# Optimization experiments

Measured on AMD Instinct MI355X. Metric: run time of the kernel, lower is better.

The kernel has to match this reference:

```python
import jax, jax.numpy as jnp
import numpy as np
import math

HIDDEN = 1024
HEADS = 16
HEAD_DIM = HIDDEN // HEADS


def setup_inputs() -> dict:
    key = jax.random.key(0)
    ks = jax.random.split(key, 9)
    s = 1.0 / math.sqrt(HIDDEN)
    x = jax.random.normal(ks[0], (4, 2048, HIDDEN), dtype=jnp.float32)
    Wq = jax.random.uniform(ks[1], (HIDDEN, HIDDEN), jnp.float32, -s, s)
    bq = jax.random.uniform(ks[2], (HIDDEN,), jnp.float32, -s, s)
    Wk = jax.random.uniform(ks[3], (HIDDEN, HIDDEN), jnp.float32, -s, s)
    bk = jax.random.uniform(ks[4], (HIDDEN,), jnp.float32, -s, s)
    Wv = jax.random.uniform(ks[5], (HIDDEN, HIDDEN), jnp.float32, -s, s)
    bv = jax.random.uniform(ks[6], (HIDDEN,), jnp.float32, -s, s)
    Wo = jax.random.uniform(ks[7], (HIDDEN, HIDDEN), jnp.float32, -s, s)
    bo = jax.random.uniform(ks[8], (HIDDEN,), jnp.float32, -s, s)
    return {"x": x, "Wq": Wq, "bq": bq, "Wk": Wk, "bk": bk,
            "Wv": Wv, "bv": bv, "Wo": Wo, "bo": bo}


def reference(x, Wq, bq, Wk, bk, Wv, bv, Wo, bo):
    B, T, D = x.shape
    H, Hd = HEADS, HEAD_DIM
    scale = 1.0 / math.sqrt(Hd)
    # projections (torch Linear: y = x @ W.T + b)
    q = (x @ Wq.T + bq).reshape(B, T, H, Hd).transpose(0, 2, 1, 3)  # [B,H,T,Hd]
    k = (x @ Wk.T + bk).reshape(B, T, H, Hd).transpose(0, 2, 1, 3)
    v = (x @ Wv.T + bv).reshape(B, T, H, Hd).transpose(0, 2, 1, 3)
    scores = jnp.einsum("bhqd,bhkd->bhqk", q, k) * scale  # [B,H,T,T]
    attn = jax.nn.softmax(scores, axis=-1)
    out = jnp.einsum("bhqk,bhkd->bhqd", attn, v)  # [B,H,T,Hd]
    out = out.transpose(0, 2, 1, 3).reshape(B, T, D)
    out = out @ Wo.T + bo
    return out.mean(axis=1)  # [B, D]
```

## Files before the change

kernel.cpp:

```cpp
#include <hip/hip_runtime.h>
#include <stdint.h>

#define HIDDEN 1024
#define HEADS 16
#define HEAD_DIM 64
#define BATCH 4
#define SEQ 2048
#define NTOK (BATCH * SEQ)

typedef __attribute__((ext_vector_type(8))) short bf16x8;
typedef __attribute__((ext_vector_type(4))) float floatx4;
typedef __attribute__((ext_vector_type(16))) float floatx16;

#define SCALE_Q 0.18033688011112042f

__device__ __forceinline__ unsigned short f2bf(float f) {
    union { float f; unsigned u; } x; x.f = f;
    unsigned r = x.u + 0x7fffu + ((x.u >> 16) & 1u);
    return (unsigned short)(r >> 16);
}

__device__ __forceinline__ float fast_exp2(float x) {
#if __has_builtin(__builtin_amdgcn_exp2f)
    return __builtin_amdgcn_exp2f(x);
#else
    return exp2f(x);
#endif
}

typedef __attribute__((address_space(3))) unsigned int lds_u32;
typedef const __attribute__((address_space(1))) unsigned int gl_u32;

__device__ __forceinline__ void async_cp16(const void* g, void* l) {
#if __has_builtin(__builtin_amdgcn_global_load_lds)
    __builtin_amdgcn_global_load_lds((gl_u32*)g, (lds_u32*)l, 16, 0, 0);
#else
    *(uint4*)((char*)l + (threadIdx.x & 63) * 16) = *(const uint4*)g;
#endif
}

__global__ __launch_bounds__(256) void conv_all(
    const float* __restrict__ x, const float* __restrict__ Wq,
    const float* __restrict__ Wk, const float* __restrict__ Wv,
    unsigned short* __restrict__ x_bf, unsigned short* __restrict__ wq_bf,
    unsigned short* __restrict__ wk_bf, unsigned short* __restrict__ wv_bf,
    float* __restrict__ accp) {
    const int blk = blockIdx.x, tid = threadIdx.x;
    const float* src;
    unsigned short* dst;
    size_t i;
    if (blk < 8192) {
        src = x; dst = x_bf; i = (size_t)blk * 256 + tid;
        if (blk < 16) accp[blk * 256 + tid] = 0.0f;
    } else {
        int r = blk - 8192;
        int s = r >> 10;
        src = (s == 0) ? Wq : (s == 1) ? Wk : Wv;
        dst = (s == 0) ? wq_bf : (s == 1) ? wk_bf : wv_bf;
        i = (size_t)(r & 1023) * 256 + tid;
    }
    float4 v = *(const float4*)(src + 4 * i);
    unsigned short o[4];
    o[0] = f2bf(v.x); o[1] = f2bf(v.y); o[2] = f2bf(v.z); o[3] = f2bf(v.w);
    *(ushort4*)(dst + 4 * i) = *(ushort4*)o;
}

__global__ __launch_bounds__(256, 3) void qkv_gemm(
    const unsigned short* __restrict__ X,
    const unsigned short* __restrict__ W0, const unsigned short* __restrict__ W1,
    const unsigned short* __restrict__ W2,
    const float* __restrict__ b0, const float* __restrict__ b1,
    const float* __restrict__ b2,
    unsigned short* __restrict__ O0, unsigned short* __restrict__ O1,
    unsigned short* __restrict__ O2) {
    __shared__ __align__(16) char smem[34816];
    unsigned short* tbuf = (unsigned short*)smem;

    const int id = blockIdx.x;
    const int mb = id & 63, nzb = id >> 6;
    const int z = nzb >> 3, nz = nzb & 7;
    const int m0 = mb * 128;
    const unsigned short* W = (z == 0) ? W0 : (z == 1) ? W1 : W2;
    const float* bias       = (z == 0) ? b0 : (z == 1) ? b1 : b2;

    const int tid = threadIdx.x, lane = tid & 63, wave = tid >> 6;
    const int wm = (wave & 1) * 64, wn = (wave >> 1) * 64;

    const int srow = lane >> 2;
    const int sxc = ((lane & 3) ^ (srow & 3)) * 8;
    const unsigned short* ga[2];
    const unsigned short* gb[2];
#pragma unroll
    for (int j = 0; j < 2; ++j) {
        ga[j] = X + (size_t)(m0 + wave * 32 + j * 16 + srow) * HIDDEN + sxc;
        gb[j] = W + (size_t)(nz * 128 + wave * 32 + j * 16 + srow) * HIDDEN + sxc;
    }

    floatx4 acc[4][4];
#pragma unroll
    for (int tm = 0; tm < 4; ++tm)
#pragma unroll
        for (int tn = 0; tn < 4; ++tn)
#pragma unroll
            for (int r = 0; r < 4; ++r) acc[tm][tn][r] = 0.f;

#pragma unroll
    for (int j = 0; j < 2; ++j) {
        async_cp16(ga[j], smem + wave * 2048 + j * 1024);
        async_cp16(gb[j], smem + 16384 + wave * 2048 + j * 1024);
        ga[j] += 32; gb[j] += 32;
    }
    __syncthreads();

    const int fr = (lane & 15) * 64 + (((lane >> 4) ^ (lane & 3)) * 16);
    for (int kt = 0; kt < 32; ++kt) {
        const int cur = kt & 1;
        if (kt < 31) {
#pragma unroll
            for (int j = 0; j < 2; ++j) {
                async_cp16(ga[j], smem + (cur ^ 1) * 8192 + wave * 2048 + j * 1024);
                async_cp16(gb[j], smem + 16384 + (cur ^ 1) * 8192 + wave * 2048 + j * 1024);
                ga[j] += 32; gb[j] += 32;
            }
        }
        const char* Ab = smem + cur * 8192;
        const char* Bb = smem + 16384 + cur * 8192;
        bf16x8 af[4], bfr[4];
#pragma unroll
        for (int t = 0; t < 4; ++t) {
            af[t]  = *(bf16x8*)(Ab + (wm + t * 16) * 64 + fr);
            bfr[t] = *(bf16x8*)(Bb + (wn + t * 16) * 64 + fr);
        }
#pragma unroll
        for (int tm = 0; tm < 4; ++tm)
#pragma unroll
            for (int tn = 0; tn < 4; ++tn)
                acc[tm][tn] = __builtin_amdgcn_mfma_f32_16x16x32_bf16(af[tm], bfr[tn], acc[tm][tn], 0, 0, 0);
        if (kt < 31) __syncthreads();
    }

    const int col = lane & 15, rbase = (lane >> 4) * 4;
    __syncthreads();
    if (z == 2) {
#pragma unroll
        for (int tm = 0; tm < 4; ++tm)
#pragma unroll
            for (int tn = 0; tn < 4; ++tn) {
                const int dr = wn + tn * 16 + col;
                const float bs = bias[nz * 128 + dr];
                const int mi0 = wm + tm * 16 + rbase;
                const int mip = (mi0 & ~12) | ((mi0 & 4) << 1) | ((mi0 & 8) >> 1);
                unsigned short vals[4];
#pragma unroll
                for (int r = 0; r < 4; ++r) vals[r] = f2bf(acc[tm][tn][r] + bs);
                *(ushort4*)&tbuf[dr * 136 + mip] = *(ushort4*)vals;
            }
        __syncthreads();
        const int dr = tid >> 1, seg = tid & 1;
        const int hh = nz * 2 + (dr >> 6), dd = dr & 63;
        const int bb = m0 >> 11, tb = (m0 & (SEQ - 1)) >> 7;
        unsigned short* dst = O2 + (((size_t)bb * HEADS + hh) * HEAD_DIM + dd) * SEQ
                                 + tb * 128 + seg * 64;
        const unsigned short* srcl = &tbuf[dr * 136 + seg * 64];
#pragma unroll
        for (int i = 0; i < 8; ++i)
            *(uint4*)(dst + i * 8) = *(const uint4*)(srcl + i * 8);
    } else {
        unsigned short* O = (z == 0) ? O0 : O1;
        const float sc = (z == 0) ? SCALE_Q : 1.0f;
#pragma unroll
        for (int tm = 0; tm < 4; ++tm)
#pragma unroll
            for (int tn = 0; tn < 4; ++tn) {
                const int nn = wn + tn * 16 + col;
                const float bs = bias[nz * 128 + nn];
                const int mi0 = wm + tm * 16 + rbase;
#pragma unroll
                for (int r = 0; r < 4; ++r)
                    tbuf[(mi0 + r) * 136 + nn] = f2bf((acc[tm][tn][r] + bs) * sc);
            }
        __syncthreads();
        const int r = tid >> 1, seg = tid & 1;
        unsigned short* dst = O + (size_t)(m0 + r) * HIDDEN + nz * 128 + seg * 64;
        const unsigned short* srcl = &tbuf[r * 136 + seg * 64];
#pragma unroll
        for (int i = 0; i < 8; ++i)
            *(uint4*)(dst + i * 8) = *(const uint4*)(srcl + i * 8);
    }
}

__global__ __launch_bounds__(256, 2) void attn_mfma(
    const unsigned short* __restrict__ Q, const unsigned short* __restrict__ K,
    const unsigned short* __restrict__ Vt, float* __restrict__ accp) {
    __shared__ unsigned short Klds[2][4096];
    __shared__ unsigned short Vlds[2][4096];

    const int tid = threadIdx.x, lane = tid & 63, wave = tid >> 6;
    const int lq = lane & 31, g2 = lane >> 5;

    const int f = blockIdx.x;
    const int bh = (f & 7) * 8 + ((f >> 3) & 7);
    const int qc = f >> 6;
    const int b = bh >> 4, h = bh & 15;

    bf16x8 qfrag[2][4];
#pragma unroll
    for (int grp = 0; grp < 2; ++grp) {
        const size_t qb = ((size_t)(b * SEQ + qc * 256 + wave * 64 + grp * 32 + lq)) * HIDDEN
                          + h * HEAD_DIM + g2 * 8;
#pragma unroll
        for (int ds = 0; ds < 4; ++ds) qfrag[grp][ds] = *(const bf16x8*)&Q[qb + ds * 16];
    }

    const unsigned short* kg[2];
    const unsigned short* vg[2];
    {
        const int kr = lane >> 3;
        const int kc = ((lane & 7) ^ kr) * 8;
#pragma unroll
        for (int j = 0; j < 2; ++j)
            kg[j] = K + ((size_t)(b * SEQ + wave * 16 + j * 8 + kr)) * HIDDEN + h * HEAD_DIM + kc;
#pragma unroll
        for (int j = 0; j < 2; ++j) {
            const int dl = wave * 16 + j * 8 + (lane >> 3);
            const int cc = ((lane & 7) ^ (dl & 7)) * 8;
            vg[j] = Vt + ((size_t)bh * HEAD_DIM + dl) * SEQ + cc;
        }
    }

    floatx16 oacc[2][2];
#pragma unroll
    for (int r = 0; r < 16; ++r) {
        oacc[0][0][r] = 0.f; oacc[0][1][r] = 0.f;
        oacc[1][0][r] = 0.f; oacc[1][1][r] = 0.f;
    }
    float lsum00 = 0.f, lsum01 = 0.f, lsum10 = 0.f, lsum11 = 0.f;

#pragma unroll
    for (int j = 0; j < 2; ++j) {
        async_cp16(kg[j], (char*)Klds[0] + (wave * 16 + j * 8) * 128);
        async_cp16(vg[j], (char*)Vlds[0] + (wave * 16 + j * 8) * 128);
        kg[j] += 64 * HIDDEN; vg[j] += 64;
    }
    __syncthreads();

    for (int it = 0; it < 32; ++it) {
        const int cur = it & 1;
        if (it < 31) {
#pragma unroll
            for (int j = 0; j < 2; ++j) {
                async_cp16(kg[j], (char*)Klds[cur ^ 1] + (wave * 16 + j * 8) * 128);
                async_cp16(vg[j], (char*)Vlds[cur ^ 1] + (wave * 16 + j * 8) * 128);
                kg[j] += 64 * HIDDEN; vg[j] += 64;
            }
        }
#pragma unroll
        for (int s32 = 0; s32 < 2; ++s32) {
            const int rr = s32 * 32 + lq;
            bf16x8 kf[4];
#pragma unroll
            for (int ds = 0; ds < 4; ++ds)
                kf[ds] = *(bf16x8*)((char*)Klds[cur] + rr * 128 + (((g2 + 2 * ds) ^ (lq & 7)) * 16));

            unsigned pk[2][8];
#pragma unroll
            for (int grp = 0; grp < 2; ++grp) {
                floatx16 sacc;
#pragma unroll
                for (int r = 0; r < 16; ++r) sacc[r] = 0.f;
                __builtin_amdgcn_s_setprio(1);
#pragma unroll
                for (int ds = 0; ds < 4; ++ds)
                    sacc = __builtin_amdgcn_mfma_f32_32x32x16_bf16(kf[ds], qfrag[grp][ds], sacc, 0, 0, 0);
                __builtin_amdgcn_s_setprio(0);

#pragma unroll
                for (int j = 0; j < 8; ++j) {
                    union { float f; unsigned u; } plo, phi;
                    plo.f = fast_exp2(sacc[2 * j]);
                    phi.f = fast_exp2(sacc[2 * j + 1]);
                    if (grp == 0) { lsum00 += plo.f; lsum01 += phi.f; }
                    else          { lsum10 += plo.f; lsum11 += phi.f; }
                    pk[grp][j] = __builtin_amdgcn_perm(phi.u, plo.u, 0x07060302u);
                }
            }
#pragma unroll
            for (int ks2 = 0; ks2 < 2; ++ks2) {
                const int s = s32 * 2 + ks2;
                bf16x8 vf[2];
#pragma unroll
                for (int nf = 0; nf < 2; ++nf) {
                    const int d = nf * 32 + lq;
                    const int c = (2 * s + g2) ^ (d & 7);
                    vf[nf] = *(bf16x8*)((char*)Vlds[cur] + d * 128 + c * 16);
                }
#pragma unroll
                for (int grp = 0; grp < 2; ++grp) {
                    union { uint4 u; bf16x8 v; } af;
                    af.u.x = pk[grp][4 * ks2];
                    af.u.y = pk[grp][4 * ks2 + 1];
                    af.u.z = pk[grp][4 * ks2 + 2];
                    af.u.w = pk[grp][4 * ks2 + 3];
                    __builtin_amdgcn_s_setprio(1);
#pragma unroll
                    for (int nf = 0; nf < 2; ++nf)
                        oacc[grp][nf] = __builtin_amdgcn_mfma_f32_32x32x16_bf16(af.v, vf[nf], oacc[grp][nf], 0, 0, 0);
                    __builtin_amdgcn_s_setprio(0);
                }
            }
        }
        if (it < 31) __syncthreads();
    }

    float linv[2][16];
#pragma unroll
    for (int grp = 0; grp < 2; ++grp) {
        float lf = (grp == 0) ? (lsum00 + lsum01) : (lsum10 + lsum11);
        lf += __shfl_xor(lf, 32, 64);
#pragma unroll
        for (int r = 0; r < 16; ++r) {
            const int qr = (r & 3) + 8 * (r >> 2) + 4 * g2;
            linv[grp][r] = 1.0f / __shfl(lf, qr, 64);
        }
    }
#pragma unroll
    for (int nf = 0; nf < 2; ++nf) {
        float v = 0.f;
#pragma unroll
        for (int r = 0; r < 16; ++r)
            v += oacc[0][nf][r] * linv[0][r] + oacc[1][nf][r] * linv[1][r];
        v += __shfl_xor(v, 32, 64);
        if (lane < 32)
            atomicAdd(&accp[b * HIDDEN + h * HEAD_DIM + nf * 32 + lq], v);
    }
}

__global__ __launch_bounds__(256) void out_proj(const float* __restrict__ acc,
                                                const float* __restrict__ Wo,
                                                const float* __restrict__ bo,
                                                float* __restrict__ out) {
    __shared__ float red[256];
    const int n = blockIdx.x * 64 + (threadIdx.x & 63);
    const int ks = threadIdx.x >> 6;
    const int b = blockIdx.y;
    const float* wr = Wo + (size_t)n * HIDDEN + ks * 256;
    const float* ar = acc + b * HIDDEN + ks * 256;
    float s = 0.f;
#pragma unroll 8
    for (int k = 0; k < 256; k += 4) {
        float4 w = *(const float4*)(wr + k);
        float4 a = *(const float4*)(ar + k);
        s += w.x * a.x + w.y * a.y + w.z * a.z + w.w * a.w;
    }
    red[threadIdx.x] = s;
    __syncthreads();
    if (threadIdx.x < 64) {
        float t = red[threadIdx.x] + red[threadIdx.x + 64]
                + red[threadIdx.x + 128] + red[threadIdx.x + 192];
        out[b * HIDDEN + n] = t * (1.0f / (float)SEQ) + bo[n];
    }
}

extern "C" void kernel_launch(void* const* d_in, const int* in_sizes, int n_in,
                              void* d_out, int out_size, void* d_ws, size_t ws_size,
                              hipStream_t stream) {
    const float* x  = (const float*)d_in[0];
    const float* Wq = (const float*)d_in[1];
    const float* bq = (const float*)d_in[2];
    const float* Wk = (const float*)d_in[3];
    const float* bk = (const float*)d_in[4];
    const float* Wv = (const float*)d_in[5];
    const float* bv = (const float*)d_in[6];
    const float* Wo = (const float*)d_in[7];
    const float* bo = (const float*)d_in[8];
    float* out = (float*)d_out;

    char* ws = (char*)d_ws;
    unsigned short* x_bf  = (unsigned short*)(ws);
    unsigned short* wq_bf = (unsigned short*)(ws + 16777216);
    unsigned short* wk_bf = (unsigned short*)(ws + 18874368);
    unsigned short* wv_bf = (unsigned short*)(ws + 20971520);
    unsigned short* q_bf  = (unsigned short*)(ws + 23068672);
    unsigned short* k_bf  = (unsigned short*)(ws + 39845888);
    unsigned short* vt_bf = (unsigned short*)(ws + 56623104);
    float*          accp  = (float*)(ws + 73400320);

    conv_all<<<dim3(8192 + 3072), dim3(256), 0, stream>>>(
        x, Wq, Wk, Wv, x_bf, wq_bf, wk_bf, wv_bf, accp);

    qkv_gemm<<<dim3(1536), dim3(256), 0, stream>>>(
        x_bf, wq_bf, wk_bf, wv_bf, bq, bk, bv, q_bf, k_bf, vt_bf);

    attn_mfma<<<dim3(512), dim3(256), 0, stream>>>(q_bf, k_bf, vt_bf, accp);

    out_proj<<<dim3(16, BATCH), dim3(256), 0, stream>>>(accp, Wo, bo, out);
}
```

Measured before the change: 250.1 us.

## Halve attention block to two waves and reorder QK/exp/PV scheduling

Attention blocks shrink from four waves to two. Each block now covers 128 query rows and the grid doubles to 1024 blocks, so each wave copies twice as many K/V rows into LDS. The inner loop is also reordered: both QK^T MFMA chains are issued back to back, the V fragments are loaded before the exponentials, and the s_setprio hints are removed. The aim is better occupancy and overlap of LDS reads and exp work with MFMAs. The cost is twice the K/V tile loading per query, because each 128-row block streams the full K/V sequence, and higher register pressure from holding two score tiles and four V fragments at once.

Measured after the change: 253.0 us. No clear change (+1.2%).

```diff
diff --git a/kernel.cpp b/kernel.cpp
--- a/kernel.cpp
+++ b/kernel.cpp
@@ -189,7 +189,7 @@
     }
 }
 
-__global__ __launch_bounds__(256, 2) void attn_mfma(
+__global__ __launch_bounds__(128, 2) void attn_mfma(
     const unsigned short* __restrict__ Q, const unsigned short* __restrict__ K,
     const unsigned short* __restrict__ Vt, float* __restrict__ accp) {
     __shared__ unsigned short Klds[2][4096];
@@ -206,23 +206,23 @@
     bf16x8 qfrag[2][4];
 #pragma unroll
     for (int grp = 0; grp < 2; ++grp) {
-        const size_t qb = ((size_t)(b * SEQ + qc * 256 + wave * 64 + grp * 32 + lq)) * HIDDEN
+        const size_t qb = ((size_t)(b * SEQ + qc * 128 + wave * 64 + grp * 32 + lq)) * HIDDEN
                           + h * HEAD_DIM + g2 * 8;
 #pragma unroll
         for (int ds = 0; ds < 4; ++ds) qfrag[grp][ds] = *(const bf16x8*)&Q[qb + ds * 16];
     }
 
-    const unsigned short* kg[2];
-    const unsigned short* vg[2];
+    const unsigned short* kg[4];
+    const unsigned short* vg[4];
     {
         const int kr = lane >> 3;
         const int kc = ((lane & 7) ^ kr) * 8;
 #pragma unroll
-        for (int j = 0; j < 2; ++j)
-            kg[j] = K + ((size_t)(b * SEQ + wave * 16 + j * 8 + kr)) * HIDDEN + h * HEAD_DIM + kc;
-#pragma unroll
-        for (int j = 0; j < 2; ++j) {
-            const int dl = wave * 16 + j * 8 + (lane >> 3);
+        for (int j = 0; j < 4; ++j)
+            kg[j] = K + ((size_t)(b * SEQ + wave * 32 + j * 8 + kr)) * HIDDEN + h * HEAD_DIM + kc;
+#pragma unroll
+        for (int j = 0; j < 4; ++j) {
+            const int dl = wave * 32 + j * 8 + (lane >> 3);
             const int cc = ((lane & 7) ^ (dl & 7)) * 8;
             vg[j] = Vt + ((size_t)bh * HEAD_DIM + dl) * SEQ + cc;
         }
@@ -237,9 +237,9 @@
     float lsum00 = 0.f, lsum01 = 0.f, lsum10 = 0.f, lsum11 = 0.f;
 
 #pragma unroll
-    for (int j = 0; j < 2; ++j) {
-        async_cp16(kg[j], (char*)Klds[0] + (wave * 16 + j * 8) * 128);
-        async_cp16(vg[j], (char*)Vlds[0] + (wave * 16 + j * 8) * 128);
+    for (int j = 0; j < 4; ++j) {
+        async_cp16(kg[j], (char*)Klds[0] + (wave * 32 + j * 8) * 128);
+        async_cp16(vg[j], (char*)Vlds[0] + (wave * 32 + j * 8) * 128);
         kg[j] += 64 * HIDDEN; vg[j] += 64;
     }
     __syncthreads();
@@ -248,9 +248,9 @@
         const int cur = it & 1;
         if (it < 31) {
 #pragma unroll
-            for (int j = 0; j < 2; ++j) {
-                async_cp16(kg[j], (char*)Klds[cur ^ 1] + (wave * 16 + j * 8) * 128);
-                async_cp16(vg[j], (char*)Vlds[cur ^ 1] + (wave * 16 + j * 8) * 128);
+            for (int j = 0; j < 4; ++j) {
+                async_cp16(kg[j], (char*)Klds[cur ^ 1] + (wave * 32 + j * 8) * 128);
+                async_cp16(vg[j], (char*)Vlds[cur ^ 1] + (wave * 32 + j * 8) * 128);
                 kg[j] += 64 * HIDDEN; vg[j] += 64;
             }
         }
@@ -262,38 +262,46 @@
             for (int ds = 0; ds < 4; ++ds)
                 kf[ds] = *(bf16x8*)((char*)Klds[cur] + rr * 128 + (((g2 + 2 * ds) ^ (lq & 7)) * 16));
 
-            unsigned pk[2][8];
-#pragma unroll
-            for (int grp = 0; grp < 2; ++grp) {
-                floatx16 sacc;
-#pragma unroll
-                for (int r = 0; r < 16; ++r) sacc[r] = 0.f;
-                __builtin_amdgcn_s_setprio(1);
-#pragma unroll
-                for (int ds = 0; ds < 4; ++ds)
-                    sacc = __builtin_amdgcn_mfma_f32_32x32x16_bf16(kf[ds], qfrag[grp][ds], sacc, 0, 0, 0);
-                __builtin_amdgcn_s_setprio(0);
-
-#pragma unroll
-                for (int j = 0; j < 8; ++j) {
-                    union { float f; unsigned u; } plo, phi;
-                    plo.f = fast_exp2(sacc[2 * j]);
-                    phi.f = fast_exp2(sacc[2 * j + 1]);
-                    if (grp == 0) { lsum00 += plo.f; lsum01 += phi.f; }
-                    else          { lsum10 += plo.f; lsum11 += phi.f; }
-                    pk[grp][j] = __builtin_amdgcn_perm(phi.u, plo.u, 0x07060302u);
-                }
-            }
-#pragma unroll
-            for (int ks2 = 0; ks2 < 2; ++ks2) {
-                const int s = s32 * 2 + ks2;
-                bf16x8 vf[2];
+            floatx16 sacc0, sacc1;
+#pragma unroll
+            for (int r = 0; r < 16; ++r) { sacc0[r] = 0.f; sacc1[r] = 0.f; }
+#pragma unroll
+            for (int ds = 0; ds < 4; ++ds)
+                sacc0 = __builtin_amdgcn_mfma_f32_32x32x16_bf16(kf[ds], qfrag[0][ds], sacc0, 0, 0, 0);
+#pragma unroll
+            for (int ds = 0; ds < 4; ++ds)
+                sacc1 = __builtin_amdgcn_mfma_f32_32x32x16_bf16(kf[ds], qfrag[1][ds], sacc1, 0, 0, 0);
+
+            bf16x8 vf[2][2];
+#pragma unroll
+            for (int ks2 = 0; ks2 < 2; ++ks2)
 #pragma unroll
                 for (int nf = 0; nf < 2; ++nf) {
                     const int d = nf * 32 + lq;
-                    const int c = (2 * s + g2) ^ (d & 7);
-                    vf[nf] = *(bf16x8*)((char*)Vlds[cur] + d * 128 + c * 16);
+                    const int c = (2 * (s32 * 2 + ks2) + g2) ^ (d & 7);
+                    vf[ks2][nf] = *(bf16x8*)((char*)Vlds[cur] + d * 128 + c * 16);
                 }
+
+            unsigned pk[2][8];
+#pragma unroll
+            for (int j = 0; j < 8; ++j) {
+                union { float f; unsigned u; } plo, phi;
+                plo.f = fast_exp2(sacc0[2 * j]);
+                phi.f = fast_exp2(sacc0[2 * j + 1]);
+                lsum00 += plo.f; lsum01 += phi.f;
+                pk[0][j] = __builtin_amdgcn_perm(phi.u, plo.u, 0x07060302u);
+            }
+#pragma unroll
+            for (int j = 0; j < 8; ++j) {
+                union { float f; unsigned u; } plo, phi;
+                plo.f = fast_exp2(sacc1[2 * j]);
+                phi.f = fast_exp2(sacc1[2 * j + 1]);
+                lsum10 += plo.f; lsum11 += phi.f;
+                pk[1][j] = __builtin_amdgcn_perm(phi.u, plo.u, 0x07060302u);
+            }
+
+#pragma unroll
+            for (int ks2 = 0; ks2 < 2; ++ks2)
 #pragma unroll
                 for (int grp = 0; grp < 2; ++grp) {
                     union { uint4 u; bf16x8 v; } af;
@@ -301,13 +309,10 @@
                     af.u.y = pk[grp][4 * ks2 + 1];
                     af.u.z = pk[grp][4 * ks2 + 2];
                     af.u.w = pk[grp][4 * ks2 + 3];
-                    __builtin_amdgcn_s_setprio(1);
 #pragma unroll
                     for (int nf = 0; nf < 2; ++nf)
-                        oacc[grp][nf] = __builtin_amdgcn_mfma_f32_32x32x16_bf16(af.v, vf[nf], oacc[grp][nf], 0, 0, 0);
-                    __builtin_amdgcn_s_setprio(0);
+                        oacc[grp][nf] = __builtin_amdgcn_mfma_f32_32x32x16_bf16(af.v, vf[ks2][nf], oacc[grp][nf], 0, 0, 0);
                 }
-            }
         }
         if (it < 31) __syncthreads();
     }
@@ -391,7 +396,7 @@
     qkv_gemm<<<dim3(1536), dim3(256), 0, stream>>>(
         x_bf, wq_bf, wk_bf, wv_bf, bq, bk, bv, q_bf, k_bf, vt_bf);
 
-    attn_mfma<<<dim3(512), dim3(256), 0, stream>>>(q_bf, k_bf, vt_bf, accp);
+    attn_mfma<<<dim3(1024), dim3(128), 0, stream>>>(q_bf, k_bf, vt_bf, accp);
 
     out_proj<<<dim3(16, BATCH), dim3(256), 0, stream>>>(accp, Wo, bo, out);
 }
```
